# Kernel tuning notes

Measured on AMD Instinct MI355X. Metric: run time of the kernel, lower is better.

The kernel has to match this reference:

```python
import jax, jax.numpy as jnp
import numpy as np

J = 1.0        # adhesion coupling
TEMP = 1.0     # Metropolis temperature
MCS_STEPS = 4  # monte-carlo sweeps per forward
N_CELL_TYPES = 16


def setup_inputs() -> dict:
    key = jax.random.key(0)
    k1, k2, k3, k4 = jax.random.split(key, 4)
    B, C, H, W = 8, 8, 1024, 1024
    X = jax.random.normal(k1, (B, C, H, W), dtype=jnp.float32)
    # channel 0 is the cell-ID image: small non-negative integer labels
    ids = jax.random.randint(k2, (B, H, W), 0, N_CELL_TYPES).astype(jnp.float32)
    X = X.at[:, 0].set(ids)
    conv_w = jax.random.normal(k3, (4, C), dtype=jnp.float32) * 0.1  # 1x1 conv: C -> 4
    conv_b = jax.random.normal(k4, (4,), dtype=jnp.float32) * 0.1
    return {"X": X, "conv_w": conv_w, "conv_b": conv_b}


def _neighbors(ids):
    # (B,H,W) -> (B,H,W,4): up, down, left, right via periodic roll
    return jnp.stack([
        jnp.roll(ids, (-1, 0), (-2, -1)),
        jnp.roll(ids, (1, 0), (-2, -1)),
        jnp.roll(ids, (0, -1), (-2, -1)),
        jnp.roll(ids, (0, 1), (-2, -1)),
    ], axis=-1)


def _cpm_forward(X, conv_w, conv_b):
    B, C, H, W = X.shape
    # 1x1 conv producing per-direction NN energy term dH_NN: (B,H,W,4)
    dH_NN = jnp.einsum('bchw,oc->bhwo', X, conv_w) + conv_b
    ids = X[:, 0]
    yy = jnp.arange(H)[:, None]
    xx = jnp.arange(W)[None, :]
    parity = ((yy + xx) % 2).astype(jnp.int32)  # checkerboard decomposition

    keys = jax.random.split(jax.random.key(42), 2 * MCS_STEPS)
    subs = jnp.tile(jnp.array([0, 1], jnp.int32), MCS_STEPS)

    def half_step(ids, carry):
        k, sub = carry
        k1, k2 = jax.random.split(k)
        dirs = jax.random.randint(k1, (B, H, W), 0, 4)            # random flip-source direction
        nb = _neighbors(ids)                                       # (B,H,W,4)
        src = jnp.take_along_axis(nb, dirs[..., None], -1)[..., 0]
        # local adhesion dH: J * (unlike-neighbor count after flip - before)
        dH_adh = J * (jnp.sum(nb != src[..., None], -1)
                      - jnp.sum(nb != ids[..., None], -1)).astype(ids.dtype)
        dH_nn = jnp.take_along_axis(dH_NN, dirs[..., None], -1)[..., 0]
        dH = dH_adh + dH_nn
        u = jax.random.uniform(k2, (B, H, W))
        accept = (u < jnp.exp(-dH / TEMP)) & (parity == sub)
        return jnp.where(accept, src, ids), None

    ids, _ = jax.lax.scan(half_step, ids, (keys, subs))
    return X.at[:, 0].set(ids)


def reference(X, conv_w, conv_b):
    return _cpm_forward(X, conv_w, conv_b)
```

## Files before the change

kernel.cpp:

```cpp
#include <hip/hip_runtime.h>
#include <stdint.h>


#define HW    1048576
#define BHWu  8388608u
#define NHu   4194304u

struct KeysK { uint32_t d[8][2]; uint32_t u[8][2]; };

__device__ __host__ __forceinline__ void tf2x32(uint32_t k0, uint32_t k1,
                                                uint32_t x0, uint32_t x1,
                                                uint32_t& o0, uint32_t& o1) {
  uint32_t k2 = k0 ^ k1 ^ 0x1BD11BDAu;
  x0 += k0; x1 += k1;
#define RDD(r) { x0 += x1; x1 = (x1 << (r)) | (x1 >> (32 - (r))); x1 ^= x0; }
  RDD(13) RDD(15) RDD(26) RDD(6)
  x0 += k1; x1 += k2 + 1u;
  RDD(17) RDD(29) RDD(16) RDD(24)
  x0 += k2; x1 += k0 + 2u;
  RDD(13) RDD(15) RDD(26) RDD(6)
  x0 += k0; x1 += k1 + 3u;
  RDD(17) RDD(29) RDD(16) RDD(24)
  x0 += k1; x1 += k2 + 4u;
  RDD(13) RDD(15) RDD(26) RDD(6)
  x0 += k2; x1 += k0 + 5u;
#undef RDD
  o0 = x0; o1 = x1;
}

__device__ __forceinline__ float xla_expf(float input) {
  float x  = fmaxf(fminf(input, 88.3762626647950f), -88.3762626647949f);
  float fx = floorf(fmaf(x, 1.44269504088896341f, 0.5f));
  float tmp = __fmul_rn(0.693359375f, fx);
  float z   = __fmul_rn(-2.12194440e-4f, fx);
  x = __fsub_rn(x, tmp);
  x = __fsub_rn(x, z);
  z = __fmul_rn(x, x);
  float y = fmaf(x, 1.9875691500e-4f, 1.3981999507e-3f);
  y = fmaf(y, x, 8.3334519073e-3f);
  y = fmaf(y, x, 4.1665795894e-2f);
  y = fmaf(y, x, 1.6666665459e-1f);
  y = fmaf(y, x, 5.0000001201e-1f);
  y = fmaf(y, z, x);
  y = __fadd_rn(y, 1.0f);
  int n = (int)fx;
  float p2n = __int_as_float((n + 127) << 23);
  return fmaxf(__fmul_rn(y, p2n), input);
}

#define BY(v, i) ((uint32_t)(((v) >> ((i) * 8)) & 0xffu))
#define ACC_D(dd) (u < xla_expf(-__fadd_rn((float)(dd), v)))

__global__ __launch_bounds__(256) void prep_fused(const float* __restrict__ X,
                                                  const float* __restrict__ W,
                                                  const float* __restrict__ Bb,
                                                  uint8_t* __restrict__ code,
                                                  uint8_t* __restrict__ ids,
                                                  float* __restrict__ out,
                                                  KeysK K) {
  const uint32_t tid = threadIdx.x;
  const uint32_t g = blockIdx.x, group = g / 15u, r = g - group * 15u;
  if (r >= 8u) {
    uint32_t j = group * 7u + (r - 8u);
    const float4* X4 = (const float4*)X;
    float4*       O4 = (float4*)out;
#pragma unroll
    for (uint32_t i = 0; i < 16u; i++) {
      uint32_t F = j * 4096u + i * 256u + tid;
      uint32_t b = F / 1835008u;
      uint32_t rem = F - b * 1835008u;
      size_t idx = ((size_t)b << 21) + 262144u + rem;
      O4[idx] = X4[idx];
    }
    return;
  }
  const uint32_t cb    = group * 8u + r;
  const uint32_t lane  = tid & 127u;
  const uint32_t rhalf = tid >> 7;
  const uint32_t row   = cb * 2u + rhalf;
  const uint32_t b = row >> 10, y = row & 1023u;
  const uint32_t ylsb = y & 1u;

  const float4* xb = (const float4*)(X + ((size_t)b << 23));
  const uint32_t fq = (y << 8) + 2u * lane;

  float acc[8][4];
  float x0[8];
#pragma unroll
  for (int c = 0; c < 8; c++) {
    float4 a  = xb[((uint32_t)c << 18) + fq];
    float4 bv = xb[((uint32_t)c << 18) + fq + 1u];
    float xs[8] = {a.x, a.y, a.z, a.w, bv.x, bv.y, bv.z, bv.w};
    if (c == 0) {
#pragma unroll
      for (int px = 0; px < 8; px++) x0[px] = xs[px];
    }
#pragma unroll
    for (int px = 0; px < 8; px++)
#pragma unroll
      for (int o = 0; o < 4; o++) {
        float m = __fmul_rn(xs[px], W[o * 8 + c]);
        acc[px][o] = (c == 0) ? __fadd_rn(0.0f, m) : __fadd_rn(acc[px][o], m);
      }
  }
#pragma unroll
  for (int px = 0; px < 8; px++)
#pragma unroll
    for (int o = 0; o < 4; o++) acc[px][o] = __fadd_rn(acc[px][o], Bb[o]);

  {
    uint32_t lo = ((uint32_t)(uint8_t)(int)x0[0])
                | ((uint32_t)(uint8_t)(int)x0[1] << 8)
                | ((uint32_t)(uint8_t)(int)x0[2] << 16)
                | ((uint32_t)(uint8_t)(int)x0[3] << 24);
    uint32_t hi = ((uint32_t)(uint8_t)(int)x0[4])
                | ((uint32_t)(uint8_t)(int)x0[5] << 8)
                | ((uint32_t)(uint8_t)(int)x0[6] << 16)
                | ((uint32_t)(uint8_t)(int)x0[7] << 24);
    uint2 v2 = {lo, hi};
    *(uint2*)(ids + (b << 20) + (y << 10) + 8u * lane) = v2;
  }

  const uint32_t pbase   = (b << 20) | (y << 10);
  const uint32_t codeoff = (b << 19) | (y << 9) | (4u * lane);
#pragma unroll
  for (int js = 0; js < 4; js++) {
#pragma unroll
    for (int pb = 0; pb < 2; pb++) {
      uint32_t s0 = ylsb ^ (uint32_t)pb;
      uint32_t dka = s0 ? K.d[2 * js + 1][0] : K.d[2 * js][0];
      uint32_t dkb = s0 ? K.d[2 * js + 1][1] : K.d[2 * js][1];
      uint32_t uka = s0 ? K.u[2 * js + 1][0] : K.u[2 * js][0];
      uint32_t ukb = s0 ? K.u[2 * js + 1][1] : K.u[2 * js][1];
      uint32_t cword = 0;
#pragma unroll
      for (int k = 0; k < 4; k++) {
        int px = 2 * k + pb;
        uint32_t p = pbase | (8u * lane + (uint32_t)px);
        uint32_t o0, o1, q0, q1;
        tf2x32(dka, dkb, 0u, p, o0, o1);
        uint32_t dir = (o0 ^ o1) & 3u;
        tf2x32(uka, ukb, 0u, p, q0, q1);
        uint32_t ub = (q0 ^ q1) >> 9;
        float u = __fsub_rn(__uint_as_float(ub | 0x3F800000u), 1.0f);
        float v = (dir == 0) ? acc[px][0] : (dir == 1) ? acc[px][1]
                : (dir == 2) ? acc[px][2] : acc[px][3];
        int dstar;
        if (ub == 0u) {
          dstar = 4;
        } else {
          float l2  = __log2f(u);
          float tau = fmaf(-0.693147180559945f, l2, -v);
          float gf  = floorf(tau);
          float fr  = tau - gf;
          int   gi  = (int)fmaxf(fminf(gf, 6.0f), -7.0f);
          dstar = gi;
          if (fr < 1e-4f)        dstar = ACC_D(gi)     ? gi     : gi - 1;
          else if (fr > 0.9999f) dstar = ACC_D(gi + 1) ? gi + 1 : gi;
        }
        dstar = dstar < -5 ? -5 : (dstar > 4 ? 4 : dstar);
        cword |= (uint32_t)((uint32_t)(dstar + 5) | (dir << 4)) << (8 * k);
      }
      uint32_t t = 2u * (uint32_t)js + s0;
      *(uint32_t*)(code + (size_t)t * NHu + codeoff) = cword;
    }
  }
}

template <int LAST>
__global__ __launch_bounds__(256) void step_d(uint8_t* __restrict__ ids,
                                              const uint8_t* __restrict__ codeT,
                                              float* __restrict__ out,
                                              int subi) {
  uint32_t n   = blockIdx.x * 256u + (uint32_t)threadIdx.x;
  uint32_t sub = (uint32_t)subi;
  uint32_t b   = n >> 17;
  uint32_t y   = (n >> 7) & 1023u;
  uint32_t c   = (y + sub) & 1u;
  uint32_t X8  = (n & 127u) << 3;
  uint32_t rowp = (b << 20) | (y << 10);
  uint32_t upp  = (b << 20) | (((y + 1u) & 1023u) << 10);
  uint32_t dnp  = (b << 20) | (((y - 1u) & 1023u) << 10);

  uint32_t cw = *(const uint32_t*)(codeT + ((b << 19) | (y << 9) | ((n & 127u) << 2)));

  uint64_t mid = *(const uint64_t*)(ids + rowp + X8);
  uint64_t up  = *(const uint64_t*)(ids + upp + X8);
  uint64_t dn  = *(const uint64_t*)(ids + dnp + X8);
  uint32_t e   = c ? (uint32_t)ids[rowp + ((X8 + 8u) & 1023u)]
                   : (uint32_t)ids[rowp + ((X8 + 1023u) & 1023u)];

  uint32_t nw[4];
#pragma unroll
  for (int k = 0; k < 4; k++) {
    uint32_t self  = c ? BY(mid, 2 * k + 1) : BY(mid, 2 * k);
    uint32_t left  = c ? BY(mid, 2 * k)
                       : ((k == 0) ? e : BY(mid, 2 * k - 1));
    uint32_t right = c ? ((k == 3) ? e : BY(mid, 2 * k + 2))
                       : BY(mid, 2 * k + 1);
    uint32_t n0 = c ? BY(up, 2 * k + 1) : BY(up, 2 * k);
    uint32_t n1 = c ? BY(dn, 2 * k + 1) : BY(dn, 2 * k);

    uint32_t bk  = (cw >> (8 * k)) & 0xffu;
    uint32_t dir = (bk >> 4) & 3u;
    uint32_t ds5 = bk & 15u;
    uint32_t s  = (dir == 0) ? n0 : (dir == 1) ? n1 : (dir == 2) ? right : left;
    int dadh = ((int)(n0 != s) + (int)(n1 != s) + (int)(right != s) + (int)(left != s))
             - ((int)(n0 != self) + (int)(n1 != self) + (int)(right != self) + (int)(left != self));
    nw[k] = ((uint32_t)(dadh + 5) <= ds5) ? s : self;
  }

  if (!LAST) {
    uint64_t A = (uint64_t)nw[0] | ((uint64_t)nw[1] << 16)
               | ((uint64_t)nw[2] << 32) | ((uint64_t)nw[3] << 48);
    uint64_t mask = 0x00FF00FF00FF00FFull << (8u * c);
    uint64_t nm = (mid & ~mask) | (A << (8u * c));
    *(uint64_t*)(ids + rowp + X8) = nm;
  } else {
    float f[8];
#pragma unroll
    for (int j = 0; j < 8; j++) {
      uint32_t bj = (((uint32_t)j & 1u) == c) ? nw[j >> 1] : BY(mid, j);
      f[j] = (float)bj;
    }
    float4 f0 = {f[0], f[1], f[2], f[3]};
    float4 f1 = {f[4], f[5], f[6], f[7]};
    float* op = out + ((size_t)b << 23) + (y << 10) + X8;
    *(float4*)op       = f0;
    *(float4*)(op + 4) = f1;
  }
}

__device__ __forceinline__ void metro_one(uint32_t u, uint32_t sub,
                                          uint8_t* __restrict__ ids,
                                          const float* __restrict__ dHNN,
                                          uint32_t dk0, uint32_t dk1,
                                          uint32_t uk0, uint32_t uk1) {
  uint32_t b = u >> 19;
  uint32_t r = u & 524287u;
  uint32_t y = r >> 9;
  uint32_t i = r & 511u;
  uint32_t x = (i << 1) | ((y + sub) & 1u);
  uint32_t p = (b << 20) | (y << 10) | x;
  float4 dnn = ((const float4*)dHNN)[sub * NHu + u];
  uint32_t d0, d1, u0, u1;
  tf2x32(dk0, dk1, 0u, p, d0, d1);
  uint32_t db = d0 ^ d1;
  tf2x32(uk0, uk1, 0u, p, u0, u1);
  uint32_t ub = u0 ^ u1;
  int   dir = (int)(db & 3u);
  float uu  = __fsub_rn(__uint_as_float((ub >> 9) | 0x3F800000u), 1.0f);
  uint32_t yN = (y + 1) & 1023u, yP = (y - 1) & 1023u;
  uint32_t xN = (x + 1) & 1023u, xP = (x - 1) & 1023u;
  uint32_t base = b << 20;
  uint32_t cc = ids[p];
  uint32_t n0 = ids[base + (yN << 10) + x];
  uint32_t n1 = ids[base + (yP << 10) + x];
  uint32_t n2 = ids[base + (y << 10) + xN];
  uint32_t n3 = ids[base + (y << 10) + xP];
  uint32_t s  = (dir == 0) ? n0 : (dir == 1) ? n1 : (dir == 2) ? n2 : n3;
  float dH_nn = (dir == 0) ? dnn.x : (dir == 1) ? dnn.y : (dir == 2) ? dnn.z : dnn.w;
  int dadh = ((int)(n0 != s) + (int)(n1 != s) + (int)(n2 != s) + (int)(n3 != s))
           - ((int)(n0 != cc) + (int)(n1 != cc) + (int)(n2 != cc) + (int)(n3 != cc));
  float dH = __fadd_rn((float)dadh, dH_nn);
  if (uu < xla_expf(-dH)) ids[p] = (uint8_t)s;
}

__global__ __launch_bounds__(256) void prep4_fb(const float* __restrict__ X,
                                                const float* __restrict__ W,
                                                const float* __restrict__ Bb,
                                                float* __restrict__ dHNN,
                                                uint8_t* __restrict__ ids) {
  int tid = blockIdx.x * 256 + threadIdx.x;
  int e   = tid << 2;
  int b   = e >> 20;
  int yx  = e & (HW - 1);
  int y   = yx >> 10;
  int x0  = yx & 1023;
  int q4  = yx >> 2;
  const float4* xb = (const float4*)(X + ((size_t)b << 23));
  float4 xc[8];
#pragma unroll
  for (int c = 0; c < 8; c++) xc[c] = xb[(c << 18) + q4];
#pragma unroll
  for (int j = 0; j < 4; j++) {
    float4 r;
#pragma unroll
    for (int o = 0; o < 4; o++) {
      float acc = 0.0f;
#pragma unroll
      for (int c = 0; c < 8; c++)
        acc = __fadd_rn(acc, __fmul_rn(((const float*)&xc[c])[j], W[o * 8 + c]));
      ((float*)&r)[o] = __fadd_rn(acc, Bb[o]);
    }
    int xj = x0 + j;
    ((float4*)dHNN)[((xj + y) & 1) * NHu + (uint32_t)((b << 19) | (y << 9) | (xj >> 1))] = r;
  }
  uchar4 v;
  v.x = (uint8_t)(int)xc[0].x; v.y = (uint8_t)(int)xc[0].y;
  v.z = (uint8_t)(int)xc[0].z; v.w = (uint8_t)(int)xc[0].w;
  *(uchar4*)(ids + e) = v;
}

__global__ __launch_bounds__(256) void half_step_fb(uint8_t* __restrict__ ids,
                                                    const float* __restrict__ dHNN,
                                                    uint32_t dk0, uint32_t dk1,
                                                    uint32_t uk0, uint32_t uk1,
                                                    int sub) {
  uint32_t u = blockIdx.x * 256u + threadIdx.x;
  metro_one(u, (uint32_t)sub, ids, dHNN, dk0, dk1, uk0, uk1);
}

__global__ __launch_bounds__(256) void finalize_full_fb(const float* __restrict__ X,
                                                        const uint8_t* __restrict__ ids,
                                                        float* __restrict__ out) {
  int t = blockIdx.x * 256 + threadIdx.x;
  int e = t << 2;
  int c = (e >> 20) & 7;
  float4 r;
  if (c == 0) {
    int b  = e >> 23;
    int yx = e & (HW - 1);
    uchar4 v = *(const uchar4*)(ids + ((size_t)b << 20) + yx);
    r.x = (float)v.x; r.y = (float)v.y; r.z = (float)v.z; r.w = (float)v.w;
  } else {
    r = ((const float4*)X)[t];
  }
  ((float4*)out)[t] = r;
}

extern "C" void kernel_launch(void* const* d_in, const int* in_sizes, int n_in,
                              void* d_out, int out_size, void* d_ws, size_t ws_size,
                              hipStream_t stream) {
  const float* X  = (const float*)d_in[0];
  const float* W  = (const float*)d_in[1];
  const float* Bb = (const float*)d_in[2];
  float* out = (float*)d_out;

  const size_t CODE_BYTES = (size_t)NHu * 8u;
  const size_t IDS_BYTES  = (size_t)BHWu;

  uint32_t bk0 = 0u, bk1 = 42u;
  uint32_t keys[8][2];
  for (uint32_t t = 0; t < 8; t++)
    tf2x32(bk0, bk1, 0u, t, keys[t][0], keys[t][1]);
  uint32_t K[8][4];
  KeysK KK;
  for (int t = 0; t < 8; t++) {
    uint32_t k1a, k1b;
    tf2x32(keys[t][0], keys[t][1], 0u, 0u, k1a, k1b);
    tf2x32(keys[t][0], keys[t][1], 0u, 1u, K[t][2], K[t][3]);
    tf2x32(k1a, k1b, 0u, 1u, K[t][0], K[t][1]);
    KK.d[t][0] = K[t][0]; KK.d[t][1] = K[t][1];
    KK.u[t][0] = K[t][2]; KK.u[t][1] = K[t][3];
  }

  bool ws_ok = ws_size >= CODE_BYTES + IDS_BYTES;
  if (ws_ok) {
    uint8_t* code = (uint8_t*)d_ws;
    uint8_t* ids  = (uint8_t*)d_ws + CODE_BYTES;

    prep_fused<<<7680, 256, 0, stream>>>(X, W, Bb, code, ids, out, KK);
    for (int t = 0; t < 7; t++)
      step_d<0><<<4096, 256, 0, stream>>>(ids, code + (size_t)t * NHu, out, t & 1);
    step_d<1><<<4096, 256, 0, stream>>>(ids, code + (size_t)7 * NHu, out, 1);
  } else {
    float*   dHNN = out;
    uint8_t* ids  = (uint8_t*)d_ws;
    prep4_fb<<<8192, 256, 0, stream>>>(X, W, Bb, dHNN, ids);
    for (int t = 0; t < 8; t++)
      half_step_fb<<<16384, 256, 0, stream>>>(ids, dHNN,
          K[t][0], K[t][1], K[t][2], K[t][3], t & 1);
    finalize_full_fb<<<65536, 256, 0, stream>>>(X, ids, out);
  }
  (void)in_sizes; (void)n_in; (void)out_size;
}
```

Measured before the change: 262.4 us.

## Fuse eight Metropolis half-steps into one tiled kernel with halo in LDS

```diff
diff --git a/kernel.cpp b/kernel.cpp
--- a/kernel.cpp
+++ b/kernel.cpp
@@ -5,6 +5,11 @@
 #define HW    1048576
 #define BHWu  8388608u
 #define NHu   4194304u
+
+#define TY 64
+#define TX 128
+#define RY 80
+#define RX 144
 
 struct KeysK { uint32_t d[8][2]; uint32_t u[8][2]; };
 
@@ -123,7 +128,7 @@
 
   const uint32_t pbase   = (b << 20) | (y << 10);
   const uint32_t codeoff = (b << 19) | (y << 9) | (4u * lane);
-#pragma unroll
+#pragma unroll 1
   for (int js = 0; js < 4; js++) {
 #pragma unroll
     for (int pb = 0; pb < 2; pb++) {
@@ -167,67 +172,66 @@
   }
 }
 
-template <int LAST>
-__global__ __launch_bounds__(256) void step_d(uint8_t* __restrict__ ids,
-                                              const uint8_t* __restrict__ codeT,
-                                              float* __restrict__ out,
-                                              int subi) {
-  uint32_t n   = blockIdx.x * 256u + (uint32_t)threadIdx.x;
-  uint32_t sub = (uint32_t)subi;
-  uint32_t b   = n >> 17;
-  uint32_t y   = (n >> 7) & 1023u;
-  uint32_t c   = (y + sub) & 1u;
-  uint32_t X8  = (n & 127u) << 3;
-  uint32_t rowp = (b << 20) | (y << 10);
-  uint32_t upp  = (b << 20) | (((y + 1u) & 1023u) << 10);
-  uint32_t dnp  = (b << 20) | (((y - 1u) & 1023u) << 10);
-
-  uint32_t cw = *(const uint32_t*)(codeT + ((b << 19) | (y << 9) | ((n & 127u) << 2)));
-
-  uint64_t mid = *(const uint64_t*)(ids + rowp + X8);
-  uint64_t up  = *(const uint64_t*)(ids + upp + X8);
-  uint64_t dn  = *(const uint64_t*)(ids + dnp + X8);
-  uint32_t e   = c ? (uint32_t)ids[rowp + ((X8 + 8u) & 1023u)]
-                   : (uint32_t)ids[rowp + ((X8 + 1023u) & 1023u)];
-
-  uint32_t nw[4];
-#pragma unroll
-  for (int k = 0; k < 4; k++) {
-    uint32_t self  = c ? BY(mid, 2 * k + 1) : BY(mid, 2 * k);
-    uint32_t left  = c ? BY(mid, 2 * k)
-                       : ((k == 0) ? e : BY(mid, 2 * k - 1));
-    uint32_t right = c ? ((k == 3) ? e : BY(mid, 2 * k + 2))
-                       : BY(mid, 2 * k + 1);
-    uint32_t n0 = c ? BY(up, 2 * k + 1) : BY(up, 2 * k);
-    uint32_t n1 = c ? BY(dn, 2 * k + 1) : BY(dn, 2 * k);
-
-    uint32_t bk  = (cw >> (8 * k)) & 0xffu;
-    uint32_t dir = (bk >> 4) & 3u;
-    uint32_t ds5 = bk & 15u;
-    uint32_t s  = (dir == 0) ? n0 : (dir == 1) ? n1 : (dir == 2) ? right : left;
-    int dadh = ((int)(n0 != s) + (int)(n1 != s) + (int)(right != s) + (int)(left != s))
-             - ((int)(n0 != self) + (int)(n1 != self) + (int)(right != self) + (int)(left != self));
-    nw[k] = ((uint32_t)(dadh + 5) <= ds5) ? s : self;
-  }
-
-  if (!LAST) {
-    uint64_t A = (uint64_t)nw[0] | ((uint64_t)nw[1] << 16)
-               | ((uint64_t)nw[2] << 32) | ((uint64_t)nw[3] << 48);
-    uint64_t mask = 0x00FF00FF00FF00FFull << (8u * c);
-    uint64_t nm = (mid & ~mask) | (A << (8u * c));
-    *(uint64_t*)(ids + rowp + X8) = nm;
-  } else {
-    float f[8];
-#pragma unroll
-    for (int j = 0; j < 8; j++) {
-      uint32_t bj = (((uint32_t)j & 1u) == c) ? nw[j >> 1] : BY(mid, j);
-      f[j] = (float)bj;
-    }
-    float4 f0 = {f[0], f[1], f[2], f[3]};
-    float4 f1 = {f[4], f[5], f[6], f[7]};
-    float* op = out + ((size_t)b << 23) + (y << 10) + X8;
-    *(float4*)op       = f0;
-    *(float4*)(op + 4) = f1;
+__global__ __launch_bounds__(256) void fused_steps(const uint8_t* __restrict__ ids,
+                                                   const uint8_t* __restrict__ code,
+                                                   float* __restrict__ out) {
+  __shared__ uint8_t T[RY * RX];
+  const uint32_t tid = threadIdx.x;
+  const uint32_t blk = blockIdx.x;
+  const uint32_t b  = blk >> 7;
+  const uint32_t yt = (blk >> 3) & 15u;
+  const uint32_t xt = blk & 7u;
+  const uint32_t y0 = yt * TY, x0 = xt * TX;
+
+  for (uint32_t i = tid; i < RY * RX; i += 256u) {
+    uint32_t lr = i / RX, lc = i - lr * RX;
+    uint32_t gy = (y0 + lr - 8u) & 1023u;
+    uint32_t gx = (x0 + lc - 8u) & 1023u;
+    T[i] = ids[(b << 20) | (gy << 10) | gx];
+  }
+  __syncthreads();
+
+#pragma unroll 1
+  for (int t = 0; t < 8; t++) {
+    const uint32_t rmin = 1u + (uint32_t)t, rmax = 78u - (uint32_t)t;
+    const uint32_t cmin = 1u + (uint32_t)t, cmax = 142u - (uint32_t)t;
+    const uint32_t rows = rmax - rmin + 1u;
+    const uint8_t* cp = code + (size_t)t * NHu;
+    for (uint32_t k = tid; k < rows * 71u; k += 256u) {
+      uint32_t dr = k / 71u;
+      uint32_t j  = k - dr * 71u;
+      uint32_t lr = rmin + dr;
+      uint32_t need = ((uint32_t)t + y0 + x0 + lr) & 1u;
+      uint32_t lc0  = cmin + ((cmin ^ need) & 1u);
+      uint32_t lc   = lc0 + 2u * j;
+      if (lc > cmax) continue;
+      uint32_t idx = lr * RX + lc;
+      uint32_t self = T[idx];
+      uint32_t n0 = T[idx + RX];
+      uint32_t n1 = T[idx - RX];
+      uint32_t rt = T[idx + 1];
+      uint32_t lf = T[idx - 1];
+      uint32_t gy = (y0 + lr - 8u) & 1023u;
+      uint32_t gx = (x0 + lc - 8u) & 1023u;
+      uint32_t bk = cp[(b << 19) | (gy << 9) | (gx >> 1)];
+      uint32_t dir = (bk >> 4) & 3u;
+      uint32_t ds5 = bk & 15u;
+      uint32_t s = (dir == 0) ? n0 : (dir == 1) ? n1 : (dir == 2) ? rt : lf;
+      int dadh = ((int)(n0 != s) + (int)(n1 != s) + (int)(rt != s) + (int)(lf != s))
+               - ((int)(n0 != self) + (int)(n1 != self) + (int)(rt != self) + (int)(lf != self));
+      if ((uint32_t)(dadh + 5) <= ds5) T[idx] = (uint8_t)s;
+    }
+    __syncthreads();
+  }
+
+  float* ob = out + ((size_t)b << 23);
+  for (uint32_t k = tid; k < (TY * TX / 4); k += 256u) {
+    uint32_t row = k >> 5;
+    uint32_t q   = k & 31u;
+    uint32_t idx = (8u + row) * RX + 8u + 4u * q;
+    float4 f = { (float)T[idx], (float)T[idx + 1],
+                 (float)T[idx + 2], (float)T[idx + 3] };
+    ((float4*)(ob + ((y0 + row) << 10) + x0))[q] = f;
   }
 }
 
@@ -361,9 +365,7 @@
     uint8_t* ids  = (uint8_t*)d_ws + CODE_BYTES;
 
     prep_fused<<<7680, 256, 0, stream>>>(X, W, Bb, code, ids, out, KK);
-    for (int t = 0; t < 7; t++)
-      step_d<0><<<4096, 256, 0, stream>>>(ids, code + (size_t)t * NHu, out, t & 1);
-    step_d<1><<<4096, 256, 0, stream>>>(ids, code + (size_t)7 * NHu, out, 1);
+    fused_steps<<<1024, 256, 0, stream>>>(ids, code, out);
   } else {
     float*   dHNN = out;
     uint8_t* ids  = (uint8_t*)d_ws;
```

After: 287.8 us. 1.1x slower.
